# Kernel tuning notes

Measured on AMD Instinct MI355X. Metric: run time of the kernel, lower is better.

Reference implementation:

```python
import jax, jax.numpy as jnp
import numpy as np

D_MODEL = 512
MAX_LEN = 1024
N_BATCH = 128
N_PART = 512


def make_encoding(d_model, max_len):
    pos = np.arange(max_len, dtype=np.float32)[:, None]            # [L,1]
    _2i = np.arange(0, d_model, 2, dtype=np.float32)[None, :]      # [1,D/2]
    angle = pos / np.power(10000.0, _2i / d_model)                 # [L,D/2]
    enc = np.zeros((max_len, d_model), dtype=np.float32)
    enc[:, 0::2] = np.sin(angle)
    enc[:, 1::2] = np.cos(angle)
    return jnp.asarray(enc)


def setup_inputs() -> dict:
    key = jax.random.key(0)
    k1, k2, k3, k4, k5 = jax.random.split(key, 5)
    dfn = jax.random.randint(k1, (N_BATCH, N_PART), 0, MAX_LEN, dtype=jnp.int64)
    dfn_fa = jax.random.randint(k2, (N_BATCH, N_PART), 0, MAX_LEN, dtype=jnp.int64)
    latent = jax.random.normal(k3, (N_BATCH, N_PART, D_MODEL), dtype=jnp.float32)
    # Linear(2*d_model -> d_model), torch default init scale ~1/sqrt(fan_in)
    bound = 1.0 / np.sqrt(2 * D_MODEL)
    W = jax.random.uniform(k4, (2 * D_MODEL, D_MODEL), jnp.float32, -bound, bound)
    b = jax.random.uniform(k5, (D_MODEL,), jnp.float32, -bound, bound)
    encoding = make_encoding(D_MODEL, MAX_LEN)
    return {"dfn": dfn, "dfn_fa": dfn_fa, "tokenized_parts_latent": latent,
            "encoding": encoding, "W": W, "b": b}


def reference(dfn, dfn_fa, tokenized_parts_latent, encoding, W, b):
    # gather position embeddings for node and parent DFS numbers, add
    pos_emb = encoding[dfn] + encoding[dfn_fa]                     # [B,P,D]
    x = jnp.concatenate([pos_emb, tokenized_parts_latent], axis=-1)  # [B,P,2D]
    out = jnp.einsum('bpk,kd->bpd', x, W) + b                      # [B,P,D]
    return out
```

## Files before the change

kernel.cpp:

```cpp
#include <hip/hip_runtime.h>
#include <hip/hip_bf16.h>
#include <stdint.h>

typedef float f32x4 __attribute__((ext_vector_type(4)));
typedef short short8 __attribute__((ext_vector_type(8)));

#define D_MODEL 512
#define MAX_LEN 1024
#define M_TOTAL 65536

static __device__ __forceinline__ short f2bf(float f) {
  union { __hip_bfloat16 h; short s; } u;
  u.h = __float2bfloat16(f);
  return u.s;
}

static __device__ __forceinline__ void gload_lds16(const void* g, void* l) {
  __builtin_amdgcn_global_load_lds(
      (const __attribute__((address_space(1))) uint32_t*)(uintptr_t)g,
      (__attribute__((address_space(3))) uint32_t*)(uint32_t)(uintptr_t)l,
      16, 0, 0);
}

static __device__ __forceinline__ void mfma_bf16(f32x4& c, short8 a, short8 b) {
  asm("v_mfma_f32_16x16x32_bf16 %0, %1, %2, %0" : "+v"(c) : "v"(a), "v"(b));
}

__global__ __launch_bounds__(256) void prep_w_kernel(const float* __restrict__ W,
                                                     short* __restrict__ WtT,
                                                     short* __restrict__ WbT) {
  __shared__ float tile[64][65];
  const int t = threadIdx.x;
  const int nt = blockIdx.x * 64;
  const int kt = blockIdx.y * 64;
  const int c = t & 63;
  const int r0 = t >> 6;
#pragma unroll
  for (int r = r0; r < 64; r += 4)
    tile[r][c] = W[(size_t)(kt + r) * D_MODEL + nt + c];
  __syncthreads();
  short* dst = (kt < D_MODEL) ? WtT : WbT;
  const int kb = kt & (D_MODEL - 1);
#pragma unroll
  for (int n = r0; n < 64; n += 4)
    dst[(size_t)(nt + n) * D_MODEL + kb + c] = f2bf(tile[c][n]);
}

__global__ __launch_bounds__(256) void prep_enc_kernel(const float* __restrict__ enc,
                                                       short* __restrict__ encb) {
  const int i = (blockIdx.x * 256 + threadIdx.x) * 4;
  float4 v = *reinterpret_cast<const float4*>(enc + i);
  short4 r = make_short4(f2bf(v.x), f2bf(v.y), f2bf(v.z), f2bf(v.w));
  *reinterpret_cast<short4*>(encb + i) = r;
}

__global__ __launch_bounds__(256) void gemm_encw_kernel(const short* __restrict__ A,
                                                        const short* __restrict__ BT,
                                                        float* __restrict__ C) {
  __shared__ short As[128 * 32];
  __shared__ short Bs[128 * 32];
  const int t = threadIdx.x;
  const int lane = t & 63;
  const int wave = t >> 6;
  const int wm = wave >> 1, wn = wave & 1;
  const int m0 = blockIdx.y * 128, n0 = blockIdx.x * 128;
  const int koff = (t & 3) * 8;
  const int rr = t >> 2;
  const int l15 = lane & 15, lk = (lane >> 4) * 8;
  f32x4 acc[4][4] = {};
  for (int kt = 0; kt < D_MODEL; kt += 32) {
    __syncthreads();
    gload_lds16(A + (size_t)(m0 + rr) * D_MODEL + kt + koff, (char*)As + t * 16);
    gload_lds16(A + (size_t)(m0 + 64 + rr) * D_MODEL + kt + koff, (char*)As + 4096 + t * 16);
    gload_lds16(BT + (size_t)(n0 + rr) * D_MODEL + kt + koff, (char*)Bs + t * 16);
    gload_lds16(BT + (size_t)(n0 + 64 + rr) * D_MODEL + kt + koff, (char*)Bs + 4096 + t * 16);
    __syncthreads();
    short8 af[4], bfr[4];
#pragma unroll
    for (int mi = 0; mi < 4; ++mi)
      af[mi] = *reinterpret_cast<const short8*>(&As[(wm * 64 + mi * 16 + l15) * 32 + lk]);
#pragma unroll
    for (int ni = 0; ni < 4; ++ni)
      bfr[ni] = *reinterpret_cast<const short8*>(&Bs[(wn * 64 + ni * 16 + l15) * 32 + lk]);
#pragma unroll
    for (int mi = 0; mi < 4; ++mi)
#pragma unroll
      for (int ni = 0; ni < 4; ++ni)
        mfma_bf16(acc[mi][ni], af[mi], bfr[ni]);
  }
#pragma unroll
  for (int mi = 0; mi < 4; ++mi)
#pragma unroll
    for (int r = 0; r < 4; ++r) {
      const int row = m0 + wm * 64 + mi * 16 + (lane >> 4) * 4 + r;
#pragma unroll
      for (int ni = 0; ni < 4; ++ni) {
        const int col = n0 + wn * 64 + ni * 16 + l15;
        C[(size_t)row * D_MODEL + col] = acc[mi][ni][r];
      }
    }
}

__global__ __launch_bounds__(256) void gemm_main_kernel(
    const float* __restrict__ latent,
    const short* __restrict__ BT,
    const float* __restrict__ encW,
    const int* __restrict__ dfn,
    const int* __restrict__ dfa,
    const float* __restrict__ bias,
    float* __restrict__ out) {
  __shared__ short As[128 * 64];
  __shared__ short Bs[128 * 64];
  const int t = threadIdx.x;
  const int lane = t & 63;
  const int wave = t >> 6;
  const int wm = wave >> 1, wn = wave & 1;

  const int bid = blockIdx.x;
  const int slot = bid >> 3;
  const int mblk = (bid & 7) * 64 + (slot >> 2);
  const int nblk = slot & 3;
  const int m0 = mblk * 128, n0 = nblk * 128;

  const int rbb = t >> 3;
  const int sb = t & 7;
  const int ra = t >> 1;
  const int ha = t & 1;

  const int l15 = lane & 15;
  const int lsl = lane >> 4;

  f32x4 acc[4][4] = {};

  for (int kt = 0; kt < D_MODEL; kt += 64) {
    __syncthreads();
#pragma unroll
    for (int c = 0; c < 4; ++c) {
      const int r = c * 32 + rbb;
      const int sg = sb ^ (r & 7);
      gload_lds16(BT + (size_t)(n0 + r) * D_MODEL + kt + sg * 8,
                  (char*)Bs + c * 4096 + t * 16);
    }
    const float4* asrc =
        reinterpret_cast<const float4*>(latent + (size_t)(m0 + ra) * D_MODEL + kt + ha * 32);
    float4 av[8];
#pragma unroll
    for (int j = 0; j < 8; ++j) av[j] = asrc[j];
#pragma unroll
    for (int j = 0; j < 4; ++j) {
      short8 h8;
      h8[0] = f2bf(av[2 * j].x); h8[1] = f2bf(av[2 * j].y);
      h8[2] = f2bf(av[2 * j].z); h8[3] = f2bf(av[2 * j].w);
      h8[4] = f2bf(av[2 * j + 1].x); h8[5] = f2bf(av[2 * j + 1].y);
      h8[6] = f2bf(av[2 * j + 1].z); h8[7] = f2bf(av[2 * j + 1].w);
      const int sw = (ha * 4 + j) ^ (ra & 7);
      *reinterpret_cast<short8*>((char*)As + ra * 128 + sw * 16) = h8;
    }
    __syncthreads();
#pragma unroll
    for (int kk = 0; kk < 2; ++kk) {
      short8 af[4], bfr[4];
#pragma unroll
      for (int mi = 0; mi < 4; ++mi) {
        const int r = wm * 64 + mi * 16 + l15;
        const int s = (kk * 4 + lsl) ^ (r & 7);
        af[mi] = *reinterpret_cast<const short8*>((char*)As + r * 128 + s * 16);
      }
#pragma unroll
      for (int ni = 0; ni < 4; ++ni) {
        const int r = wn * 64 + ni * 16 + l15;
        const int s = (kk * 4 + lsl) ^ (r & 7);
        bfr[ni] = *reinterpret_cast<const short8*>((char*)Bs + r * 128 + s * 16);
      }
#pragma unroll
      for (int mi = 0; mi < 4; ++mi)
#pragma unroll
        for (int ni = 0; ni < 4; ++ni)
          mfma_bf16(acc[mi][ni], af[mi], bfr[ni]);
    }
  }

#pragma unroll
  for (int mi = 0; mi < 4; ++mi) {
#pragma unroll
    for (int r = 0; r < 4; ++r) {
      const int row = m0 + wm * 64 + mi * 16 + (lane >> 4) * 4 + r;
      const int d1 = dfn[row];
      const int d2 = dfa[row];
      const float* e1 = encW + (size_t)d1 * D_MODEL;
      const float* e2 = encW + (size_t)d2 * D_MODEL;
      const size_t ro = (size_t)row * D_MODEL;
#pragma unroll
      for (int ni = 0; ni < 4; ++ni) {
        const int col = n0 + wn * 64 + ni * 16 + l15;
        out[ro + col] = acc[mi][ni][r] + e1[col] + e2[col] + bias[col];
      }
    }
  }
}

extern "C" void kernel_launch(void* const* d_in, const int* in_sizes, int n_in,
                              void* d_out, int out_size, void* d_ws, size_t ws_size,
                              hipStream_t stream) {
  const int* dfn = (const int*)d_in[0];
  const int* dfa = (const int*)d_in[1];
  const float* latent = (const float*)d_in[2];
  const float* enc = (const float*)d_in[3];
  const float* W = (const float*)d_in[4];
  const float* bias = (const float*)d_in[5];
  float* out = (float*)d_out;

  char* ws = (char*)d_ws;
  short* WtT  = (short*)(ws);
  short* WbT  = (short*)(ws + 512 * 1024);
  short* encb = (short*)(ws + 1024 * 1024);
  float* encW = (float*)(ws + 2 * 1024 * 1024);

  hipLaunchKernelGGL(prep_w_kernel, dim3(8, 16), dim3(256), 0, stream, W, WtT, WbT);
  hipLaunchKernelGGL(prep_enc_kernel, dim3(512), dim3(256), 0, stream, enc, encb);
  hipLaunchKernelGGL(gemm_encw_kernel, dim3(4, 8), dim3(256), 0, stream, encb, WtT, encW);
  hipLaunchKernelGGL(gemm_main_kernel, dim3(2048), dim3(256), 0, stream,
                     latent, WbT, encW, dfn, dfa, bias, out);
}
```

Measured before the change: 133.2 us.

## Load GEMM operands directly from global into registers, dropping LDS staging

The main GEMM kernel no longer stages A and B tiles through shared memory with barriers. Each wave loads its own MFMA fragments straight from global memory into registers, converting fp32 latent to bf16 in-register, and double-buffers the 32-wide k slices so loads overlap compute. This removes LDS traffic and syncthreads, but each block now reads every A and B row twice across waves with less coalesced 32-byte/16-byte accesses, relying on L1/L2 for reuse.

```diff
diff --git a/kernel.cpp b/kernel.cpp
--- a/kernel.cpp
+++ b/kernel.cpp
@@ -4,6 +4,7 @@
 
 typedef float f32x4 __attribute__((ext_vector_type(4)));
 typedef short short8 __attribute__((ext_vector_type(8)));
+typedef __bf16 bf16x8 __attribute__((ext_vector_type(8)));
 
 #define D_MODEL 512
 #define MAX_LEN 1024
@@ -13,6 +14,12 @@
   union { __hip_bfloat16 h; short s; } u;
   u.h = __float2bfloat16(f);
   return u.s;
+}
+
+static __device__ __forceinline__ bf16x8 as_bf16x8(short8 s) {
+  union { short8 s; bf16x8 b; } u;
+  u.s = s;
+  return u.b;
 }
 
 static __device__ __forceinline__ void gload_lds16(const void* g, void* l) {
@@ -101,6 +108,44 @@
     }
 }
 
+static __device__ __forceinline__ void load_slice(const float* const (&ap)[4],
+                                                  const short* const (&bp)[4],
+                                                  int ko,
+                                                  f32x4 (&alo)[4], f32x4 (&ahi)[4],
+                                                  short8 (&bv)[4]) {
+#pragma unroll
+  for (int mi = 0; mi < 4; ++mi) {
+    alo[mi] = *reinterpret_cast<const f32x4*>(ap[mi] + ko);
+    ahi[mi] = *reinterpret_cast<const f32x4*>(ap[mi] + ko + 4);
+  }
+#pragma unroll
+  for (int ni = 0; ni < 4; ++ni)
+    bv[ni] = *reinterpret_cast<const short8*>(bp[ni] + ko);
+}
+
+static __device__ __forceinline__ void compute_step(f32x4 (&acc)[4][4],
+                                                    const f32x4 (&alo)[4],
+                                                    const f32x4 (&ahi)[4],
+                                                    const short8 (&bv)[4]) {
+  bf16x8 af[4], bfv[4];
+#pragma unroll
+  for (int mi = 0; mi < 4; ++mi) {
+    short8 h;
+    h[0] = f2bf(alo[mi][0]); h[1] = f2bf(alo[mi][1]);
+    h[2] = f2bf(alo[mi][2]); h[3] = f2bf(alo[mi][3]);
+    h[4] = f2bf(ahi[mi][0]); h[5] = f2bf(ahi[mi][1]);
+    h[6] = f2bf(ahi[mi][2]); h[7] = f2bf(ahi[mi][3]);
+    af[mi] = as_bf16x8(h);
+  }
+#pragma unroll
+  for (int ni = 0; ni < 4; ++ni) bfv[ni] = as_bf16x8(bv[ni]);
+#pragma unroll
+  for (int mi = 0; mi < 4; ++mi)
+#pragma unroll
+    for (int ni = 0; ni < 4; ++ni)
+      acc[mi][ni] = __builtin_amdgcn_mfma_f32_16x16x32_bf16(af[mi], bfv[ni], acc[mi][ni], 0, 0, 0);
+}
+
 __global__ __launch_bounds__(256) void gemm_main_kernel(
     const float* __restrict__ latent,
     const short* __restrict__ BT,
@@ -109,8 +154,6 @@
     const int* __restrict__ dfa,
     const float* __restrict__ bias,
     float* __restrict__ out) {
-  __shared__ short As[128 * 64];
-  __shared__ short Bs[128 * 64];
   const int t = threadIdx.x;
   const int lane = t & 63;
   const int wave = t >> 6;
@@ -122,69 +165,38 @@
   const int nblk = slot & 3;
   const int m0 = mblk * 128, n0 = nblk * 128;
 
-  const int rbb = t >> 3;
-  const int sb = t & 7;
-  const int ra = t >> 1;
-  const int ha = t & 1;
-
-  const int l15 = lane & 15;
-  const int lsl = lane >> 4;
+  const int r15 = lane & 15;
+  const int q = lane >> 4;
+
+  const float* ap[4];
+  const short* bp[4];
+#pragma unroll
+  for (int mi = 0; mi < 4; ++mi)
+    ap[mi] = latent + (size_t)(m0 + wm * 64 + mi * 16 + r15) * D_MODEL + q * 8;
+#pragma unroll
+  for (int ni = 0; ni < 4; ++ni)
+    bp[ni] = BT + (size_t)(n0 + wn * 64 + ni * 16 + r15) * D_MODEL + q * 8;
 
   f32x4 acc[4][4] = {};
 
+  f32x4 a0l[4], a0h[4], a1l[4], a1h[4];
+  short8 b0[4], b1[4];
+  load_slice(ap, bp, 0, a0l, a0h, b0);
+
+#pragma unroll
   for (int kt = 0; kt < D_MODEL; kt += 64) {
-    __syncthreads();
-#pragma unroll
-    for (int c = 0; c < 4; ++c) {
-      const int r = c * 32 + rbb;
-      const int sg = sb ^ (r & 7);
-      gload_lds16(BT + (size_t)(n0 + r) * D_MODEL + kt + sg * 8,
-                  (char*)Bs + c * 4096 + t * 16);
-    }
-    const float4* asrc =
-        reinterpret_cast<const float4*>(latent + (size_t)(m0 + ra) * D_MODEL + kt + ha * 32);
-    float4 av[8];
-#pragma unroll
-    for (int j = 0; j < 8; ++j) av[j] = asrc[j];
-#pragma unroll
-    for (int j = 0; j < 4; ++j) {
-      short8 h8;
-      h8[0] = f2bf(av[2 * j].x); h8[1] = f2bf(av[2 * j].y);
-      h8[2] = f2bf(av[2 * j].z); h8[3] = f2bf(av[2 * j].w);
-      h8[4] = f2bf(av[2 * j + 1].x); h8[5] = f2bf(av[2 * j + 1].y);
-      h8[6] = f2bf(av[2 * j + 1].z); h8[7] = f2bf(av[2 * j + 1].w);
-      const int sw = (ha * 4 + j) ^ (ra & 7);
-      *reinterpret_cast<short8*>((char*)As + ra * 128 + sw * 16) = h8;
-    }
-    __syncthreads();
-#pragma unroll
-    for (int kk = 0; kk < 2; ++kk) {
-      short8 af[4], bfr[4];
-#pragma unroll
-      for (int mi = 0; mi < 4; ++mi) {
-        const int r = wm * 64 + mi * 16 + l15;
-        const int s = (kk * 4 + lsl) ^ (r & 7);
-        af[mi] = *reinterpret_cast<const short8*>((char*)As + r * 128 + s * 16);
-      }
-#pragma unroll
-      for (int ni = 0; ni < 4; ++ni) {
-        const int r = wn * 64 + ni * 16 + l15;
-        const int s = (kk * 4 + lsl) ^ (r & 7);
-        bfr[ni] = *reinterpret_cast<const short8*>((char*)Bs + r * 128 + s * 16);
-      }
-#pragma unroll
-      for (int mi = 0; mi < 4; ++mi)
-#pragma unroll
-        for (int ni = 0; ni < 4; ++ni)
-          mfma_bf16(acc[mi][ni], af[mi], bfr[ni]);
-    }
+    load_slice(ap, bp, kt + 32, a1l, a1h, b1);
+    compute_step(acc, a0l, a0h, b0);
+    if (kt + 64 < D_MODEL)
+      load_slice(ap, bp, kt + 64, a0l, a0h, b0);
+    compute_step(acc, a1l, a1h, b1);
   }
 
 #pragma unroll
   for (int mi = 0; mi < 4; ++mi) {
 #pragma unroll
     for (int r = 0; r < 4; ++r) {
-      const int row = m0 + wm * 64 + mi * 16 + (lane >> 4) * 4 + r;
+      const int row = m0 + wm * 64 + mi * 16 + q * 4 + r;
       const int d1 = dfn[row];
       const int d2 = dfa[row];
       const float* e1 = encW + (size_t)d1 * D_MODEL;
@@ -192,7 +204,7 @@
       const size_t ro = (size_t)row * D_MODEL;
 #pragma unroll
       for (int ni = 0; ni < 4; ++ni) {
-        const int col = n0 + wn * 64 + ni * 16 + l15;
+        const int col = n0 + wn * 64 + ni * 16 + r15;
         out[ro + col] = acc[mi][ni][r] + e1[col] + e2[col] + bias[col];
       }
     }
```

New measurement: 248.2 us. 86.3% more time.

## Double-buffer LDS tiles in main GEMM to overlap loads with MFMA

Applied to the files above, without the earlier changes.

The main GEMM kernel now uses two LDS buffers each for A and B and prefetches the next k-tile (B via direct global-to-LDS loads, A via register loads) while MFMAs run on the current tile, with one barrier per step instead of two. The inline-asm MFMA is replaced by the compiler builtin, which lets the compiler schedule around it, and launch bounds now ask for 2 blocks per CU. The cost is twice the LDS (64KB per block) and more live registers for the prefetched A values, which may limit occupancy.

```diff
diff --git a/kernel.cpp b/kernel.cpp
--- a/kernel.cpp
+++ b/kernel.cpp
@@ -4,6 +4,7 @@
 
 typedef float f32x4 __attribute__((ext_vector_type(4)));
 typedef short short8 __attribute__((ext_vector_type(8)));
+typedef __bf16 bf16x8 __attribute__((ext_vector_type(8)));
 
 #define D_MODEL 512
 #define MAX_LEN 1024
@@ -13,6 +14,12 @@
   union { __hip_bfloat16 h; short s; } u;
   u.h = __float2bfloat16(f);
   return u.s;
+}
+
+static __device__ __forceinline__ bf16x8 as_bf16x8(short8 s) {
+  union { short8 s; bf16x8 b; } u;
+  u.s = s;
+  return u.b;
 }
 
 static __device__ __forceinline__ void gload_lds16(const void* g, void* l) {
@@ -101,7 +108,7 @@
     }
 }
 
-__global__ __launch_bounds__(256) void gemm_main_kernel(
+__global__ __launch_bounds__(256, 2) void gemm_main_kernel(
     const float* __restrict__ latent,
     const short* __restrict__ BT,
     const float* __restrict__ encW,
@@ -109,8 +116,10 @@
     const int* __restrict__ dfa,
     const float* __restrict__ bias,
     float* __restrict__ out) {
-  __shared__ short As[128 * 64];
-  __shared__ short Bs[128 * 64];
+  __shared__ alignas(16) short As0[128 * 64];
+  __shared__ alignas(16) short As1[128 * 64];
+  __shared__ alignas(16) short Bs0[128 * 64];
+  __shared__ alignas(16) short Bs1[128 * 64];
   const int t = threadIdx.x;
   const int lane = t & 63;
   const int wave = t >> 6;
@@ -130,53 +139,87 @@
   const int l15 = lane & 15;
   const int lsl = lane >> 4;
 
+  const float* aptr = latent + (size_t)(m0 + ra) * D_MODEL + ha * 32;
+  const short* bptr[4];
+#pragma unroll
+  for (int c = 0; c < 4; ++c) {
+    const int r = c * 32 + rbb;
+    const int sg = sb ^ (r & 7);
+    bptr[c] = BT + (size_t)(n0 + r) * D_MODEL + sg * 8;
+  }
+
   f32x4 acc[4][4] = {};
-
-  for (int kt = 0; kt < D_MODEL; kt += 64) {
-    __syncthreads();
-#pragma unroll
-    for (int c = 0; c < 4; ++c) {
-      const int r = c * 32 + rbb;
-      const int sg = sb ^ (r & 7);
-      gload_lds16(BT + (size_t)(n0 + r) * D_MODEL + kt + sg * 8,
-                  (char*)Bs + c * 4096 + t * 16);
-    }
-    const float4* asrc =
-        reinterpret_cast<const float4*>(latent + (size_t)(m0 + ra) * D_MODEL + kt + ha * 32);
-    float4 av[8];
-#pragma unroll
-    for (int j = 0; j < 8; ++j) av[j] = asrc[j];
-#pragma unroll
-    for (int j = 0; j < 4; ++j) {
-      short8 h8;
-      h8[0] = f2bf(av[2 * j].x); h8[1] = f2bf(av[2 * j].y);
-      h8[2] = f2bf(av[2 * j].z); h8[3] = f2bf(av[2 * j].w);
-      h8[4] = f2bf(av[2 * j + 1].x); h8[5] = f2bf(av[2 * j + 1].y);
-      h8[6] = f2bf(av[2 * j + 1].z); h8[7] = f2bf(av[2 * j + 1].w);
-      const int sw = (ha * 4 + j) ^ (ra & 7);
-      *reinterpret_cast<short8*>((char*)As + ra * 128 + sw * 16) = h8;
-    }
-    __syncthreads();
-#pragma unroll
-    for (int kk = 0; kk < 2; ++kk) {
-      short8 af[4], bfr[4];
-#pragma unroll
-      for (int mi = 0; mi < 4; ++mi) {
-        const int r = wm * 64 + mi * 16 + l15;
-        const int s = (kk * 4 + lsl) ^ (r & 7);
-        af[mi] = *reinterpret_cast<const short8*>((char*)As + r * 128 + s * 16);
+  float4 av[8];
+
+#define STAGE_B(KO, BDST)                                                   \
+  {                                                                         \
+    _Pragma("unroll") for (int c = 0; c < 4; ++c)                           \
+        gload_lds16(bptr[c] + (KO), (char*)(BDST) + c * 4096 + t * 16);     \
+  }
+#define LOAD_A(KO)                                                          \
+  {                                                                         \
+    const float4* s4 = reinterpret_cast<const float4*>(aptr + (KO));        \
+    _Pragma("unroll") for (int j = 0; j < 8; ++j) av[j] = s4[j];            \
+  }
+#define WRITE_A(ADST)                                                       \
+  {                                                                         \
+    _Pragma("unroll") for (int j = 0; j < 4; ++j) {                         \
+      short8 h8;                                                            \
+      h8[0] = f2bf(av[2 * j].x); h8[1] = f2bf(av[2 * j].y);                 \
+      h8[2] = f2bf(av[2 * j].z); h8[3] = f2bf(av[2 * j].w);                 \
+      h8[4] = f2bf(av[2 * j + 1].x); h8[5] = f2bf(av[2 * j + 1].y);         \
+      h8[6] = f2bf(av[2 * j + 1].z); h8[7] = f2bf(av[2 * j + 1].w);         \
+      const int sw = (ha * 4 + j) ^ (ra & 7);                               \
+      *reinterpret_cast<short8*>((char*)(ADST) + ra * 128 + sw * 16) = h8;  \
+    }                                                                       \
+  }
+#define COMPUTE(ASRC, BSRC)                                                 \
+  {                                                                         \
+    _Pragma("unroll") for (int kk = 0; kk < 2; ++kk) {                      \
+      bf16x8 af[4], bfv[4];                                                 \
+      _Pragma("unroll") for (int mi = 0; mi < 4; ++mi) {                    \
+        const int r = wm * 64 + mi * 16 + l15;                              \
+        const int s = (kk * 4 + lsl) ^ (r & 7);                             \
+        af[mi] = as_bf16x8(                                                 \
+            *reinterpret_cast<const short8*>((char*)(ASRC) + r * 128 + s * 16)); \
+      }                                                                     \
+      _Pragma("unroll") for (int ni = 0; ni < 4; ++ni) {                    \
+        const int r = wn * 64 + ni * 16 + l15;                              \
+        const int s = (kk * 4 + lsl) ^ (r & 7);                             \
+        bfv[ni] = as_bf16x8(                                                \
+            *reinterpret_cast<const short8*>((char*)(BSRC) + r * 128 + s * 16)); \
+      }                                                                     \
+      _Pragma("unroll") for (int mi = 0; mi < 4; ++mi)                      \
+          _Pragma("unroll") for (int ni = 0; ni < 4; ++ni)                  \
+              acc[mi][ni] = __builtin_amdgcn_mfma_f32_16x16x32_bf16(        \
+                  af[mi], bfv[ni], acc[mi][ni], 0, 0, 0);                   \
+    }                                                                       \
+  }
+
+  STAGE_B(0, Bs0);
+  LOAD_A(0);
+  WRITE_A(As0);
+  __syncthreads();
+
+#pragma unroll
+  for (int tt = 0; tt < 4; ++tt) {
+    {
+      const int ko = (2 * tt + 1) * 64;
+      STAGE_B(ko, Bs1);
+      LOAD_A(ko);
+      COMPUTE(As0, Bs0);
+      WRITE_A(As1);
+      __syncthreads();
+    }
+    {
+      if (tt < 3) {
+        const int ko = (2 * tt + 2) * 64;
+        STAGE_B(ko, Bs0);
+        LOAD_A(ko);
       }
-#pragma unroll
-      for (int ni = 0; ni < 4; ++ni) {
-        const int r = wn * 64 + ni * 16 + l15;
-        const int s = (kk * 4 + lsl) ^ (r & 7);
-        bfr[ni] = *reinterpret_cast<const short8*>((char*)Bs + r * 128 + s * 16);
-      }
-#pragma unroll
-      for (int mi = 0; mi < 4; ++mi)
-#pragma unroll
-        for (int ni = 0; ni < 4; ++ni)
-          mfma_bf16(acc[mi][ni], af[mi], bfr[ni]);
+      COMPUTE(As1, Bs1);
+      if (tt < 3) WRITE_A(As0);
+      __syncthreads();
     }
   }
 
@@ -184,7 +227,7 @@
   for (int mi = 0; mi < 4; ++mi) {
 #pragma unroll
     for (int r = 0; r < 4; ++r) {
-      const int row = m0 + wm * 64 + mi * 16 + (lane >> 4) * 4 + r;
+      const int row = m0 + wm * 64 + mi * 16 + lsl * 4 + r;
       const int d1 = dfn[row];
       const int d2 = dfa[row];
       const float* e1 = encW + (size_t)d1 * D_MODEL;
@@ -197,6 +240,10 @@
       }
     }
   }
+#undef STAGE_B
+#undef LOAD_A
+#undef WRITE_A
+#undef COMPUTE
 }
 
 extern "C" void kernel_launch(void* const* d_in, const int* in_sizes, int n_in,
```

Result: slower. 142.4 us (+6.8%).

## Load fp32 latent directly into LDS via async copies, convert at fragment read

Applied to the files above, without the earlier changes.

The main GEMM now streams the fp32 latent tile straight into LDS with global_load_lds instead of loading through registers and converting before the store. Conversion to bf16 moves to the point where MFMA fragments are read from LDS. The K step drops from 64 to 32 with new XOR swizzles, and the MFMA call switches from inline asm to the builtin, which lets the compiler schedule around it. Launch bounds now ask for 4 blocks per CU. The cost is more loop iterations and barriers, and each tile is converted redundantly by both waves that read it.

```diff
diff --git a/kernel.cpp b/kernel.cpp
--- a/kernel.cpp
+++ b/kernel.cpp
@@ -4,6 +4,7 @@
 
 typedef float f32x4 __attribute__((ext_vector_type(4)));
 typedef short short8 __attribute__((ext_vector_type(8)));
+typedef __bf16 bf16x8 __attribute__((ext_vector_type(8)));
 
 #define D_MODEL 512
 #define MAX_LEN 1024
@@ -13,6 +14,12 @@
   union { __hip_bfloat16 h; short s; } u;
   u.h = __float2bfloat16(f);
   return u.s;
+}
+
+static __device__ __forceinline__ bf16x8 as_bf16x8(short8 s) {
+  union { short8 s; bf16x8 b; } u;
+  u.s = s;
+  return u.b;
 }
 
 static __device__ __forceinline__ void gload_lds16(const void* g, void* l) {
@@ -101,7 +108,7 @@
     }
 }
 
-__global__ __launch_bounds__(256) void gemm_main_kernel(
+__global__ __launch_bounds__(256, 4) void gemm_main_kernel(
     const float* __restrict__ latent,
     const short* __restrict__ BT,
     const float* __restrict__ encW,
@@ -109,8 +116,8 @@
     const int* __restrict__ dfa,
     const float* __restrict__ bias,
     float* __restrict__ out) {
-  __shared__ short As[128 * 64];
-  __shared__ short Bs[128 * 64];
+  __shared__ alignas(16) float Af[128 * 32];
+  __shared__ alignas(16) short Bs[128 * 32];
   const int t = threadIdx.x;
   const int lane = t & 63;
   const int wave = t >> 6;
@@ -122,69 +129,67 @@
   const int nblk = slot & 3;
   const int m0 = mblk * 128, n0 = nblk * 128;
 
-  const int rbb = t >> 3;
-  const int sb = t & 7;
-  const int ra = t >> 1;
-  const int ha = t & 1;
-
   const int l15 = lane & 15;
   const int lsl = lane >> 4;
 
+  const int arow = t >> 3;
+  const int acol = ((t & 7) ^ (arow & 7)) * 4;
+  const float* aSrc[4];
+#pragma unroll
+  for (int p = 0; p < 4; ++p)
+    aSrc[p] = latent + (size_t)(m0 + p * 32 + arow) * D_MODEL + acol;
+
+  const int brow = t >> 2;
+  const int bcol = ((t & 3) ^ ((t >> 3) & 3)) * 8;
+  const short* bSrc[2];
+#pragma unroll
+  for (int p = 0; p < 2; ++p)
+    bSrc[p] = BT + (size_t)(n0 + p * 64 + brow) * D_MODEL + bcol;
+
   f32x4 acc[4][4] = {};
 
-  for (int kt = 0; kt < D_MODEL; kt += 64) {
-    __syncthreads();
-#pragma unroll
-    for (int c = 0; c < 4; ++c) {
-      const int r = c * 32 + rbb;
-      const int sg = sb ^ (r & 7);
-      gload_lds16(BT + (size_t)(n0 + r) * D_MODEL + kt + sg * 8,
-                  (char*)Bs + c * 4096 + t * 16);
-    }
-    const float4* asrc =
-        reinterpret_cast<const float4*>(latent + (size_t)(m0 + ra) * D_MODEL + kt + ha * 32);
-    float4 av[8];
-#pragma unroll
-    for (int j = 0; j < 8; ++j) av[j] = asrc[j];
-#pragma unroll
-    for (int j = 0; j < 4; ++j) {
-      short8 h8;
-      h8[0] = f2bf(av[2 * j].x); h8[1] = f2bf(av[2 * j].y);
-      h8[2] = f2bf(av[2 * j].z); h8[3] = f2bf(av[2 * j].w);
-      h8[4] = f2bf(av[2 * j + 1].x); h8[5] = f2bf(av[2 * j + 1].y);
-      h8[6] = f2bf(av[2 * j + 1].z); h8[7] = f2bf(av[2 * j + 1].w);
-      const int sw = (ha * 4 + j) ^ (ra & 7);
-      *reinterpret_cast<short8*>((char*)As + ra * 128 + sw * 16) = h8;
-    }
-    __syncthreads();
-#pragma unroll
-    for (int kk = 0; kk < 2; ++kk) {
-      short8 af[4], bfr[4];
-#pragma unroll
-      for (int mi = 0; mi < 4; ++mi) {
-        const int r = wm * 64 + mi * 16 + l15;
-        const int s = (kk * 4 + lsl) ^ (r & 7);
-        af[mi] = *reinterpret_cast<const short8*>((char*)As + r * 128 + s * 16);
-      }
-#pragma unroll
-      for (int ni = 0; ni < 4; ++ni) {
-        const int r = wn * 64 + ni * 16 + l15;
-        const int s = (kk * 4 + lsl) ^ (r & 7);
-        bfr[ni] = *reinterpret_cast<const short8*>((char*)Bs + r * 128 + s * 16);
-      }
-#pragma unroll
-      for (int mi = 0; mi < 4; ++mi)
-#pragma unroll
-        for (int ni = 0; ni < 4; ++ni)
-          mfma_bf16(acc[mi][ni], af[mi], bfr[ni]);
-    }
+  for (int kt = 0; kt < D_MODEL; kt += 32) {
+    __syncthreads();
+#pragma unroll
+    for (int p = 0; p < 4; ++p)
+      gload_lds16(aSrc[p] + kt, (char*)Af + p * 4096 + t * 16);
+#pragma unroll
+    for (int p = 0; p < 2; ++p)
+      gload_lds16(bSrc[p] + kt, (char*)Bs + p * 4096 + t * 16);
+    __syncthreads();
+    bf16x8 af[4], bfv[4];
+#pragma unroll
+    for (int mi = 0; mi < 4; ++mi) {
+      const int r = wm * 64 + mi * 16 + l15;
+      const int s0 = (2 * lsl) ^ (r & 7);
+      const int s1 = (2 * lsl + 1) ^ (r & 7);
+      f32x4 v0 = *reinterpret_cast<const f32x4*>((const char*)Af + r * 128 + s0 * 16);
+      f32x4 v1 = *reinterpret_cast<const f32x4*>((const char*)Af + r * 128 + s1 * 16);
+      short8 h;
+      h[0] = f2bf(v0[0]); h[1] = f2bf(v0[1]); h[2] = f2bf(v0[2]); h[3] = f2bf(v0[3]);
+      h[4] = f2bf(v1[0]); h[5] = f2bf(v1[1]); h[6] = f2bf(v1[2]); h[7] = f2bf(v1[3]);
+      af[mi] = as_bf16x8(h);
+    }
+#pragma unroll
+    for (int ni = 0; ni < 4; ++ni) {
+      const int r = wn * 64 + ni * 16 + l15;
+      const int s = lsl ^ ((r >> 1) & 3);
+      bfv[ni] = as_bf16x8(
+          *reinterpret_cast<const short8*>((const char*)Bs + r * 64 + s * 16));
+    }
+#pragma unroll
+    for (int mi = 0; mi < 4; ++mi)
+#pragma unroll
+      for (int ni = 0; ni < 4; ++ni)
+        acc[mi][ni] = __builtin_amdgcn_mfma_f32_16x16x32_bf16(
+            af[mi], bfv[ni], acc[mi][ni], 0, 0, 0);
   }
 
 #pragma unroll
   for (int mi = 0; mi < 4; ++mi) {
 #pragma unroll
     for (int r = 0; r < 4; ++r) {
-      const int row = m0 + wm * 64 + mi * 16 + (lane >> 4) * 4 + r;
+      const int row = m0 + wm * 64 + mi * 16 + lsl * 4 + r;
       const int d1 = dfn[row];
       const int d2 = dfa[row];
       const float* e1 = encW + (size_t)d1 * D_MODEL;
```

After: 115.9 us. -13.0%, faster.
